# Kernel tuning notes

Hardware: AMD Instinct MI355X
Metric: run time of the kernel (lower is better)

The kernel has to match this reference:

```python
import jax, jax.numpy as jnp
import numpy as np

B, N, D, S = 128, 512, 256, 8


def setup_inputs() -> dict:
    key = jax.random.key(0)
    k1, k2, k3, k4, k5, k6, k7 = jax.random.split(key, 7)
    node_feat = jax.random.normal(k1, (B, N, D), dtype=jnp.float32)
    query = jax.random.normal(k2, (B, D), dtype=jnp.float32)
    edge_matrices = jax.random.uniform(k3, (B, N, N), dtype=jnp.float32)
    att_stack = jax.random.uniform(k4, (B, N, S), dtype=jnp.float32)
    # soft one-hot stack pointer (as produced by the controller in the original model)
    ptr_idx = jax.random.randint(k5, (B,), 1, S)
    stack_ptr = jax.nn.one_hot(ptr_idx, S, dtype=jnp.float32)
    value_mem = jnp.zeros((B, N), dtype=jnp.float32)
    W = jax.random.normal(k6, (D, D), dtype=jnp.float32) * 0.02  # nn.Linear weight [out,in]
    b = jnp.zeros((D,), dtype=jnp.float32)
    return {
        "node_feat": node_feat, "query": query, "edge_matrices": edge_matrices,
        "att_stack": att_stack, "stack_ptr": stack_ptr, "value_mem": value_mem,
        "W": W, "b": b,
    }


def reference(node_feat, query, edge_matrices, att_stack, stack_ptr, value_mem, W, b):
    # read_from_stack: weighted sum over stack depth -> key attention [B, N]
    key_attn = jnp.sum(att_stack * stack_ptr[:, None, :], axis=-1)
    # attention-weighted node feature [B, D] and adjacency row [B, N]
    key_feat = jnp.sum(node_feat * key_attn[:, :, None], axis=1)
    edge_matrix = jnp.sum(edge_matrices * key_attn[:, :, None], axis=1)
    # linear projection of key feature -> query vector [B, D]
    q = key_feat @ W.T + b
    # neighbors = node_feat * edge_matrix[..., None]; logits = neighbors @ q
    logits = jnp.einsum('bnd,bn,bd->bn', node_feat, edge_matrix, q)
    # write_to_stack with zero attention: zero out the slot under the pointer
    new_att_stack = att_stack * (1.0 - stack_ptr[:, None, :])
    # _move_ptr_bw: shift pointer toward stack bottom; bottom absorbs itself
    shifted = jnp.concatenate([stack_ptr[:, 1:], jnp.zeros((stack_ptr.shape[0], 1), stack_ptr.dtype)], axis=1)
    new_stack_ptr = shifted.at[:, 0].add(stack_ptr[:, 0])
    new_value_mem = value_mem + logits
    return (new_att_stack, new_stack_ptr, new_value_mem)
```

## Files before the change

### kernel.cpp

```cpp
#include <hip/hip_runtime.h>

#define B 128
#define N 512
#define D 256
#define S 8

__global__ void k0_stack(const float* __restrict__ att_stack,
                         const float* __restrict__ stack_ptr,
                         float* __restrict__ out_att,
                         float* __restrict__ out_sp,
                         float* __restrict__ ka) {
    const int b = blockIdx.x;
    const int tid = threadIdx.x;
    __shared__ float sp[S];
    __shared__ float omsp[S];
    if (tid < S) {
        float v = stack_ptr[b * S + tid];
        sp[tid] = v;
        omsp[tid] = 1.0f - v;
    }
    __syncthreads();
    for (int n = tid; n < N; n += blockDim.x) {
        const float4* src = reinterpret_cast<const float4*>(att_stack + ((size_t)(b * N + n)) * S);
        float4 a0 = src[0], a1 = src[1];
        float kacc = a0.x * sp[0] + a0.y * sp[1] + a0.z * sp[2] + a0.w * sp[3]
                   + a1.x * sp[4] + a1.y * sp[5] + a1.z * sp[6] + a1.w * sp[7];
        ka[b * N + n] = kacc;
        float4 o0 = make_float4(a0.x * omsp[0], a0.y * omsp[1], a0.z * omsp[2], a0.w * omsp[3]);
        float4 o1 = make_float4(a1.x * omsp[4], a1.y * omsp[5], a1.z * omsp[6], a1.w * omsp[7]);
        float4* dst = reinterpret_cast<float4*>(out_att + ((size_t)(b * N + n)) * S);
        dst[0] = o0;
        dst[1] = o1;
    }
    if (tid < S) {
        float v = (tid < S - 1) ? sp[tid + 1] : 0.0f;
        if (tid == 0) v += sp[0];
        out_sp[b * S + tid] = v;
    }
}

__global__ void kA_edge(const float* __restrict__ edge,
                        const float* __restrict__ ka,
                        float* __restrict__ em) {
    const int b = blockIdx.y;
    const int i0 = blockIdx.x * 64;
    const int tid = threadIdx.x;
    __shared__ float kal[64];
    if (tid < 64) kal[tid] = ka[b * N + i0 + tid];
    __syncthreads();
    float4 acc = make_float4(0.f, 0.f, 0.f, 0.f);
    const float4* base = reinterpret_cast<const float4*>(edge + ((size_t)b * N + i0) * N) + tid;
    #pragma unroll 8
    for (int i = 0; i < 64; ++i) {
        float4 v = base[(size_t)i * (N / 4)];
        float k = kal[i];
        acc.x += k * v.x; acc.y += k * v.y; acc.z += k * v.z; acc.w += k * v.w;
    }
    float* dst = em + b * N + tid * 4;
    unsafeAtomicAdd(dst + 0, acc.x);
    unsafeAtomicAdd(dst + 1, acc.y);
    unsafeAtomicAdd(dst + 2, acc.z);
    unsafeAtomicAdd(dst + 3, acc.w);
}

__global__ void kB_keyfeat(const float* __restrict__ node,
                           const float* __restrict__ ka,
                           float* __restrict__ kf) {
    const int b = blockIdx.y;
    const int n0 = blockIdx.x * 64;
    const int tid = threadIdx.x;
    __shared__ float kal[64];
    kal[tid] = ka[b * N + n0 + tid];
    __syncthreads();
    float4 acc = make_float4(0.f, 0.f, 0.f, 0.f);
    const float4* base = reinterpret_cast<const float4*>(node + ((size_t)b * N + n0) * D) + tid;
    #pragma unroll 8
    for (int i = 0; i < 64; ++i) {
        float4 v = base[(size_t)i * (D / 4)];
        float k = kal[i];
        acc.x += k * v.x; acc.y += k * v.y; acc.z += k * v.z; acc.w += k * v.w;
    }
    float* dst = kf + b * D + tid * 4;
    unsafeAtomicAdd(dst + 0, acc.x);
    unsafeAtomicAdd(dst + 1, acc.y);
    unsafeAtomicAdd(dst + 2, acc.z);
    unsafeAtomicAdd(dst + 3, acc.w);
}

__global__ void kC_q(const float* __restrict__ Wm,
                     const float* __restrict__ bias,
                     const float* __restrict__ kf,
                     float* __restrict__ q) {
    const int b = blockIdx.x;
    const int d = threadIdx.x;
    __shared__ float kfl[D];
    kfl[d] = kf[b * D + d];
    __syncthreads();
    float acc = bias[d];
    const float4* wrow = reinterpret_cast<const float4*>(Wm + (size_t)d * D);
    const float4* kf4 = reinterpret_cast<const float4*>(kfl);
    #pragma unroll 8
    for (int k = 0; k < D / 4; ++k) {
        float4 w = wrow[k];
        float4 f = kf4[k];
        acc += w.x * f.x + w.y * f.y + w.z * f.z + w.w * f.w;
    }
    q[b * D + d] = acc;
}

__global__ void kD_logits(const float* __restrict__ node,
                          const float* __restrict__ em,
                          const float* __restrict__ q,
                          const float* __restrict__ vm,
                          float* __restrict__ out_vm) {
    const int row0 = blockIdx.x * 32;
    const int b = row0 / N;
    const int tid = threadIdx.x;
    const int wave = tid >> 6;
    const int lane = tid & 63;
    __shared__ float ql[D];
    if (tid < D) ql[tid] = q[b * D + tid];
    __syncthreads();
    const float4 q4 = reinterpret_cast<const float4*>(ql)[lane];
    #pragma unroll
    for (int r = 0; r < 8; ++r) {
        const int row = row0 + wave * 8 + r;
        const float4 v = reinterpret_cast<const float4*>(node + (size_t)row * D)[lane];
        float s = v.x * q4.x + v.y * q4.y + v.z * q4.z + v.w * q4.w;
        #pragma unroll
        for (int off = 32; off; off >>= 1) s += __shfl_xor(s, off);
        if (lane == 0) {
            out_vm[row] = vm[row] + em[row] * s;
        }
    }
}

extern "C" void kernel_launch(void* const* d_in, const int* in_sizes, int n_in,
                              void* d_out, int out_size, void* d_ws, size_t ws_size,
                              hipStream_t stream) {
    const float* node = (const float*)d_in[0];
    const float* edge = (const float*)d_in[2];
    const float* att  = (const float*)d_in[3];
    const float* sp   = (const float*)d_in[4];
    const float* vm   = (const float*)d_in[5];
    const float* Wm   = (const float*)d_in[6];
    const float* bias = (const float*)d_in[7];

    float* out_att = (float*)d_out;
    float* out_sp  = out_att + (size_t)B * N * S;
    float* out_vm  = out_sp + (size_t)B * S;

    float* ws = (float*)d_ws;
    float* ka = ws;
    float* kf = ws + (size_t)B * N;
    float* em = kf + (size_t)B * D;
    float* q  = em + (size_t)B * N;

    hipMemsetAsync(kf, 0, (size_t)(B * D + B * N) * sizeof(float), stream);

    k0_stack<<<B, 256, 0, stream>>>(att, sp, out_att, out_sp, ka);
    kA_edge<<<dim3(N / 64, B), 128, 0, stream>>>(edge, ka, em);
    kB_keyfeat<<<dim3(N / 64, B), 64, 0, stream>>>(node, ka, kf);
    kC_q<<<B, D, 0, stream>>>(Wm, bias, kf, q);
    kD_logits<<<(B * N) / 32, 256, 0, stream>>>(node, em, q, vm, out_vm);
}
```

Measured before the change: 69.75 us.

## Fuse stack read, edge reduction and key-feature reduction into one kernel

Merges the stack kernel, the edge-matrix reduction and the key-feature reduction into a single launch. Each block recomputes its 64 key-attention values from att_stack directly instead of reading them from a workspace buffer. Blocks 0-7 handle edge rows and blocks 8-15 handle node rows and also write the new attention stack. The node path now uses 128 threads with a shared-memory reduction across two halves. This removes two kernel launches and the ka round trip through global memory, at the cost of each row of att_stack being read twice.

New measurement: 63.74 us. 8.6% less time.

```diff
diff --git a/kernel.cpp b/kernel.cpp
--- a/kernel.cpp
+++ b/kernel.cpp
@@ -5,86 +5,85 @@
 #define D 256
 #define S 8
 
-__global__ void k0_stack(const float* __restrict__ att_stack,
-                         const float* __restrict__ stack_ptr,
-                         float* __restrict__ out_att,
-                         float* __restrict__ out_sp,
-                         float* __restrict__ ka) {
-    const int b = blockIdx.x;
+__global__ __launch_bounds__(128) void k1_fused(
+    const float* __restrict__ node, const float* __restrict__ edge,
+    const float* __restrict__ att, const float* __restrict__ spi,
+    float* __restrict__ out_att, float* __restrict__ out_sp,
+    float* __restrict__ kf, float* __restrict__ em) {
+    const int b = blockIdx.y;
+    const int role = blockIdx.x;
     const int tid = threadIdx.x;
-    __shared__ float sp[S];
-    __shared__ float omsp[S];
-    if (tid < S) {
-        float v = stack_ptr[b * S + tid];
-        sp[tid] = v;
-        omsp[tid] = 1.0f - v;
+    __shared__ float sps[S];
+    __shared__ float kal[64];
+    __shared__ float4 red[64];
+    if (tid < S) sps[tid] = spi[b * S + tid];
+    __syncthreads();
+
+    if (role < 8) {
+        const int i0 = role * 64;
+        if (tid < 64) {
+            const float4* a = reinterpret_cast<const float4*>(att + ((size_t)(b * N + i0 + tid)) * S);
+            float4 a0 = a[0], a1 = a[1];
+            kal[tid] = a0.x * sps[0] + a0.y * sps[1] + a0.z * sps[2] + a0.w * sps[3]
+                     + a1.x * sps[4] + a1.y * sps[5] + a1.z * sps[6] + a1.w * sps[7];
+        }
+        __syncthreads();
+        float4 acc = make_float4(0.f, 0.f, 0.f, 0.f);
+        const float4* base = reinterpret_cast<const float4*>(edge + ((size_t)(b * N + i0)) * N) + tid;
+        #pragma unroll 8
+        for (int i = 0; i < 64; ++i) {
+            float4 v = base[(size_t)i * (N / 4)];
+            float k = kal[i];
+            acc.x += k * v.x; acc.y += k * v.y; acc.z += k * v.z; acc.w += k * v.w;
+        }
+        float* dst = em + b * N + tid * 4;
+        unsafeAtomicAdd(dst + 0, acc.x);
+        unsafeAtomicAdd(dst + 1, acc.y);
+        unsafeAtomicAdd(dst + 2, acc.z);
+        unsafeAtomicAdd(dst + 3, acc.w);
+    } else {
+        const int n0 = (role - 8) * 64;
+        if (tid < 64) {
+            const float4* a = reinterpret_cast<const float4*>(att + ((size_t)(b * N + n0 + tid)) * S);
+            float4 a0 = a[0], a1 = a[1];
+            kal[tid] = a0.x * sps[0] + a0.y * sps[1] + a0.z * sps[2] + a0.w * sps[3]
+                     + a1.x * sps[4] + a1.y * sps[5] + a1.z * sps[6] + a1.w * sps[7];
+            float4 o0 = make_float4(a0.x * (1.f - sps[0]), a0.y * (1.f - sps[1]),
+                                    a0.z * (1.f - sps[2]), a0.w * (1.f - sps[3]));
+            float4 o1 = make_float4(a1.x * (1.f - sps[4]), a1.y * (1.f - sps[5]),
+                                    a1.z * (1.f - sps[6]), a1.w * (1.f - sps[7]));
+            float4* oa = reinterpret_cast<float4*>(out_att + ((size_t)(b * N + n0 + tid)) * S);
+            oa[0] = o0;
+            oa[1] = o1;
+        }
+        if (role == 8 && tid < S) {
+            float v = (tid < S - 1) ? sps[tid + 1] : 0.0f;
+            if (tid == 0) v += sps[0];
+            out_sp[b * S + tid] = v;
+        }
+        __syncthreads();
+        const int col = tid & 63;
+        const int r0 = (tid >> 6) * 32;
+        float4 acc = make_float4(0.f, 0.f, 0.f, 0.f);
+        const float4* base = reinterpret_cast<const float4*>(node + ((size_t)(b * N + n0)) * D) + col;
+        #pragma unroll 8
+        for (int i = 0; i < 32; ++i) {
+            float4 v = base[(size_t)(r0 + i) * (D / 4)];
+            float k = kal[r0 + i];
+            acc.x += k * v.x; acc.y += k * v.y; acc.z += k * v.z; acc.w += k * v.w;
+        }
+        if (tid >= 64) red[col] = acc;
+        __syncthreads();
+        if (tid < 64) {
+            float4 o = red[col];
+            acc.x += o.x; acc.y += o.y; acc.z += o.z; acc.w += o.w;
+            float* dst = kf + b * D + col * 4;
+            unsafeAtomicAdd(dst + 0, acc.x);
+            unsafeAtomicAdd(dst + 1, acc.y);
+            unsafeAtomicAdd(dst + 2, acc.z);
+            unsafeAtomicAdd(dst + 3, acc.w);
+        }
     }
-    __syncthreads();
-    for (int n = tid; n < N; n += blockDim.x) {
-        const float4* src = reinterpret_cast<const float4*>(att_stack + ((size_t)(b * N + n)) * S);
-        float4 a0 = src[0], a1 = src[1];
-        float kacc = a0.x * sp[0] + a0.y * sp[1] + a0.z * sp[2] + a0.w * sp[3]
-                   + a1.x * sp[4] + a1.y * sp[5] + a1.z * sp[6] + a1.w * sp[7];
-        ka[b * N + n] = kacc;
-        float4 o0 = make_float4(a0.x * omsp[0], a0.y * omsp[1], a0.z * omsp[2], a0.w * omsp[3]);
-        float4 o1 = make_float4(a1.x * omsp[4], a1.y * omsp[5], a1.z * omsp[6], a1.w * omsp[7]);
-        float4* dst = reinterpret_cast<float4*>(out_att + ((size_t)(b * N + n)) * S);
-        dst[0] = o0;
-        dst[1] = o1;
-    }
-    if (tid < S) {
-        float v = (tid < S - 1) ? sp[tid + 1] : 0.0f;
-        if (tid == 0) v += sp[0];
-        out_sp[b * S + tid] = v;
-    }
-}
-
-__global__ void kA_edge(const float* __restrict__ edge,
-                        const float* __restrict__ ka,
-                        float* __restrict__ em) {
-    const int b = blockIdx.y;
-    const int i0 = blockIdx.x * 64;
-    const int tid = threadIdx.x;
-    __shared__ float kal[64];
-    if (tid < 64) kal[tid] = ka[b * N + i0 + tid];
-    __syncthreads();
-    float4 acc = make_float4(0.f, 0.f, 0.f, 0.f);
-    const float4* base = reinterpret_cast<const float4*>(edge + ((size_t)b * N + i0) * N) + tid;
-    #pragma unroll 8
-    for (int i = 0; i < 64; ++i) {
-        float4 v = base[(size_t)i * (N / 4)];
-        float k = kal[i];
-        acc.x += k * v.x; acc.y += k * v.y; acc.z += k * v.z; acc.w += k * v.w;
-    }
-    float* dst = em + b * N + tid * 4;
-    unsafeAtomicAdd(dst + 0, acc.x);
-    unsafeAtomicAdd(dst + 1, acc.y);
-    unsafeAtomicAdd(dst + 2, acc.z);
-    unsafeAtomicAdd(dst + 3, acc.w);
-}
-
-__global__ void kB_keyfeat(const float* __restrict__ node,
-                           const float* __restrict__ ka,
-                           float* __restrict__ kf) {
-    const int b = blockIdx.y;
-    const int n0 = blockIdx.x * 64;
-    const int tid = threadIdx.x;
-    __shared__ float kal[64];
-    kal[tid] = ka[b * N + n0 + tid];
-    __syncthreads();
-    float4 acc = make_float4(0.f, 0.f, 0.f, 0.f);
-    const float4* base = reinterpret_cast<const float4*>(node + ((size_t)b * N + n0) * D) + tid;
-    #pragma unroll 8
-    for (int i = 0; i < 64; ++i) {
-        float4 v = base[(size_t)i * (D / 4)];
-        float k = kal[i];
-        acc.x += k * v.x; acc.y += k * v.y; acc.z += k * v.z; acc.w += k * v.w;
-    }
-    float* dst = kf + b * D + tid * 4;
-    unsafeAtomicAdd(dst + 0, acc.x);
-    unsafeAtomicAdd(dst + 1, acc.y);
-    unsafeAtomicAdd(dst + 2, acc.z);
-    unsafeAtomicAdd(dst + 3, acc.w);
 }
 
 __global__ void kC_q(const float* __restrict__ Wm,
@@ -151,16 +150,14 @@
     float* out_vm  = out_sp + (size_t)B * S;
 
     float* ws = (float*)d_ws;
-    float* ka = ws;
-    float* kf = ws + (size_t)B * N;
+    float* kf = ws;
     float* em = kf + (size_t)B * D;
     float* q  = em + (size_t)B * N;
 
     hipMemsetAsync(kf, 0, (size_t)(B * D + B * N) * sizeof(float), stream);
 
-    k0_stack<<<B, 256, 0, stream>>>(att, sp, out_att, out_sp, ka);
-    kA_edge<<<dim3(N / 64, B), 128, 0, stream>>>(edge, ka, em);
-    kB_keyfeat<<<dim3(N / 64, B), 64, 0, stream>>>(node, ka, kf);
+    k1_fused<<<dim3(16, B), 128, 0, stream>>>(node, edge, att, sp,
+                                              out_att, out_sp, kf, em);
     kC_q<<<B, D, 0, stream>>>(Wm, bias, kf, q);
     kD_logits<<<(B * N) / 32, 256, 0, stream>>>(node, em, q, vm, out_vm);
 }
```
